# Optimization experiments

Hardware: AMD Instinct MI355X
Metric: run time of the kernel (lower is better)

Reference implementation:

```python
import jax, jax.numpy as jnp
import numpy as np


def _keras_lstm_cell(x, h_tm1, c_tm1, k, rk, b):
    # Keras LSTMCell math: gates ordered i, f, c(g), o
    z = x @ k + h_tm1 @ rk + b  # [B, 4H]
    i, f, g, o = jnp.split(z, 4, axis=-1)
    i = jax.nn.sigmoid(i)
    f = jax.nn.sigmoid(f)
    c = f * c_tm1 + i * jnp.tanh(g)
    h = jax.nn.sigmoid(o) * jnp.tanh(c)
    return h, c


def setup_inputs() -> dict:
    key = jax.random.key(0)
    k1, k2, k3, k4 = jax.random.split(key, 4)
    T, B, H, L = 30, 256, 1024, 4
    inputs = jax.random.normal(k1, (T, B, H), dtype=jnp.float32)
    # scale weights to avoid gate saturation across 30 steps
    kernel = jax.random.normal(k2, (L, H, 4 * H), dtype=jnp.float32) * 0.05
    rec_kernel = jax.random.normal(k3, (L, H, 4 * H), dtype=jnp.float32) * 0.05
    bias = jax.random.normal(k4, (L, 4 * H), dtype=jnp.float32) * 0.05
    return {"inputs": inputs, "kernel": kernel, "rec_kernel": rec_kernel, "bias": bias}


def reference(inputs, kernel, rec_kernel, bias):
    # Faithful to the TF source: it passes (c, h) where Keras expects (h, c),
    # a self-consistent swap across steps, EXCEPT `cur_input = h` actually
    # feeds the Keras cell state c to the next layer. We reproduce that.
    T, B, H = inputs.shape
    L = kernel.shape[0]
    h0 = jnp.zeros((L, B, H), dtype=inputs.dtype)  # keras hidden per layer
    c0 = jnp.zeros((L, B, H), dtype=inputs.dtype)  # keras cell per layer

    def step(carry, x_t):
        hs, cs = carry
        cur = x_t
        new_h, new_c = [], []
        for j in range(L):
            h_new, c_new = _keras_lstm_cell(cur, hs[j], cs[j], kernel[j], rec_kernel[j], bias[j])
            cur = c_new  # source feeds its "h" (== keras cell state) onward
            new_h.append(h_new)
            new_c.append(c_new)
        return (jnp.stack(new_h), jnp.stack(new_c)), cur

    (_, _), outs = jax.lax.scan(step, (h0, c0), inputs)
    return outs[-1]  # final cur_input after the last timestep, shape [B, H]
```

## Files before the change

### kernel.cpp

```cpp
#include <hip/hip_runtime.h>
#include <hip/hip_fp16.h>

typedef _Float16 half8 __attribute__((ext_vector_type(8)));
typedef float floatx4 __attribute__((ext_vector_type(4)));

#define T_STEPS 30
#define BATCH   256
#define HID     1024
#define LAYERS  4
#define N4H     4096
#define K2      2048

#define BM 128
#define BN 128
#define BKH 64
#define KITERS 16
#define ZLD 132

#define AS1(p) ((const __attribute__((address_space(1))) void*)(p))
#define AS3(p) ((__attribute__((address_space(3))) void*)(p))

__global__ void transpose_weights(const float* __restrict__ src_all,
                                  _Float16* __restrict__ wrt, int mat) {
    __shared__ float tile[2][64][65];
    const int j = blockIdx.z;
    const float* src = src_all + (size_t)j * HID * N4H;
    _Float16* dst = wrt + (size_t)j * N4H * K2 + mat * HID;
    const int c0 = blockIdx.x * 64;
    const int k0 = blockIdx.y * 128;
    const int t = threadIdx.x;
    const int c4 = (t & 15) * 4, lr = t >> 4;
    #pragma unroll
    for (int tt = 0; tt < 2; ++tt)
        #pragma unroll
        for (int i = 0; i < 4; ++i) {
            const float4 v = *(const float4*)(src + (size_t)(k0 + tt * 64 + lr + i * 16) * N4H + c0 + c4);
            volatile float* tw = &tile[tt][lr + i * 16][c4];
            tw[0] = v.x; tw[1] = v.y; tw[2] = v.z; tw[3] = v.w;
        }
    __syncthreads();
    const int kg = t & 7, cl0 = t >> 3;
    #pragma unroll
    for (int tt = 0; tt < 2; ++tt)
        #pragma unroll
        for (int i = 0; i < 2; ++i) {
            const int cp = cl0 + i * 32;
            const int c = c0 + cp;
            const int q = ((c & (HID - 1)) << 2) | (c >> 10);
            half8 v;
            #pragma unroll
            for (int jj = 0; jj < 8; ++jj)
                v[jj] = (_Float16)tile[tt][kg * 8 + jj][cp];
            *(half8*)(dst + (size_t)q * K2 + k0 + tt * 64 + kg * 8) = v;
        }
}

__global__ void cvt_inputs(const float* __restrict__ in, _Float16* __restrict__ out) {
    const size_t i = ((size_t)blockIdx.x * 256 + threadIdx.x) * 8;
    const float4 a = *(const float4*)(in + i);
    const float4 b = *(const float4*)(in + i + 4);
    half8 v;
    v[0] = (_Float16)a.x; v[1] = (_Float16)a.y; v[2] = (_Float16)a.z; v[3] = (_Float16)a.w;
    v[4] = (_Float16)b.x; v[5] = (_Float16)b.y; v[6] = (_Float16)b.z; v[7] = (_Float16)b.w;
    *(half8*)(out + i) = v;
}

__global__ __launch_bounds__(512) void lstm_diag(
    const _Float16* __restrict__ Xf,
    _Float16*       __restrict__ c_act,
    _Float16*       __restrict__ h_act,
    const _Float16* __restrict__ WRt,
    const float*    __restrict__ bias,
    float*          __restrict__ c_master,
    int diag, int packed_t, int packed_j)
{
    const int z = blockIdx.z;
    const int t = (packed_t >> (8 * z)) & 255;
    const int j = (packed_j >> (8 * z)) & 255;
    const size_t BH = (size_t)BATCH * HID;

    const _Float16* X    = (j == 0) ? (Xf + (size_t)t * BH)
                                    : (c_act + ((size_t)((diag - 1) & 1) * LAYERS + (j - 1)) * BH);
    const _Float16* Hrec = h_act + (size_t)j * BH;
    const _Float16* WR   = WRt + (size_t)j * N4H * K2;
    const float* bias_j  = bias + (size_t)j * N4H;
    float* c_m           = c_master + (size_t)j * BH;
    _Float16* c_out      = c_act + ((size_t)(diag & 1) * LAYERS + j) * BH;
    _Float16* h_out      = h_act + (size_t)j * BH;

    __shared__ __align__(16) char smem[131072];
    float* zs = (float*)smem;

    const int tid  = threadIdx.x;
    const int w    = tid >> 6, lane = tid & 63;
    const int quad = lane >> 4, l16 = lane & 15;
    const int h    = w >> 2;
    const int sp   = w & 3;
    const int mw   = (sp & 1) * 64;
    const int nw   = (sp >> 1) * 64;
    const int m0   = blockIdx.y * BM;
    const int q0   = blockIdx.x * BN;
    const int th   = tid & 255;
    const int wbase = (w & 3) * 64;

    const _Float16* Ag0 = h ? Hrec : X;
    const _Float16* Bg0 = WR + h * HID;

    floatx4 acc[4][4];
    #pragma unroll
    for (int a = 0; a < 4; ++a)
        #pragma unroll
        for (int b = 0; b < 4; ++b)
            #pragma unroll
            for (int e = 0; e < 4; ++e) acc[a][b][e] = 0.f;

#define STAGE(bufsel, kc_) do {                                                         \
        _Float16* As_ = (_Float16*)(smem + (bufsel) * 65536 + h * 32768);               \
        _Float16* Bs_ = As_ + 8192;                                                     \
        const _Float16* Agk = Ag0 + (kc_);                                              \
        const _Float16* Bgk = Bg0 + (kc_);                                              \
        _Pragma("unroll")                                                               \
        for (int i_ = 0; i_ < 4; ++i_) {                                                \
            const int slot = i_ * 256 + th;                                             \
            const int r_ = slot >> 3;                                                   \
            const int g_ = (slot & 7) ^ (r_ & 7);                                       \
            __builtin_amdgcn_global_load_lds(AS1(Agk + (size_t)(m0 + r_) * HID + g_ * 8),\
                                             AS3(As_ + (i_ * 256 + wbase) * 8), 16, 0, 0);\
        }                                                                               \
        _Pragma("unroll")                                                               \
        for (int i_ = 0; i_ < 4; ++i_) {                                                \
            const int slot = i_ * 256 + th;                                             \
            const int q_ = slot >> 3;                                                   \
            const int g_ = (slot & 7) ^ (q_ & 7);                                       \
            __builtin_amdgcn_global_load_lds(AS1(Bgk + (size_t)(q0 + q_) * K2 + g_ * 8), \
                                             AS3(Bs_ + (i_ * 256 + wbase) * 8), 16, 0, 0);\
        }                                                                               \
    } while (0)

#define COMPUTE(bufsel) do {                                                            \
        const _Float16* As_ = (const _Float16*)(smem + (bufsel) * 65536 + h * 32768);   \
        const _Float16* Bs_ = As_ + 8192;                                               \
        _Pragma("unroll")                                                               \
        for (int ks = 0; ks < 2; ++ks) {                                                \
            const int gq = ks * 4 + quad;                                               \
            half8 bfrag[4];                                                             \
            _Pragma("unroll")                                                           \
            for (int b = 0; b < 4; ++b) {                                               \
                const int q = nw + b * 16 + l16;                                        \
                bfrag[b] = *(const half8*)&Bs_[((q << 3) + (gq ^ (q & 7))) * 8];        \
            }                                                                           \
            _Pragma("unroll")                                                           \
            for (int a = 0; a < 4; ++a) {                                               \
                const int r = mw + a * 16 + l16;                                        \
                const half8 afrag = *(const half8*)&As_[((r << 3) + (gq ^ (r & 7))) * 8];\
                acc[a][0] = __builtin_amdgcn_mfma_f32_16x16x32_f16(afrag, bfrag[0], acc[a][0], 0, 0, 0);\
                acc[a][1] = __builtin_amdgcn_mfma_f32_16x16x32_f16(afrag, bfrag[1], acc[a][1], 0, 0, 0);\
                acc[a][2] = __builtin_amdgcn_mfma_f32_16x16x32_f16(afrag, bfrag[2], acc[a][2], 0, 0, 0);\
                acc[a][3] = __builtin_amdgcn_mfma_f32_16x16x32_f16(afrag, bfrag[3], acc[a][3], 0, 0, 0);\
            }                                                                           \
        }                                                                               \
    } while (0)

    STAGE(0, 0);
    __syncthreads();
    #pragma unroll 2
    for (int ts = 0; ts < KITERS; ++ts) {
        const int cur = ts & 1;
        if (ts + 1 < KITERS) STAGE(cur ^ 1, (ts + 1) * BKH);
        COMPUTE(cur);
        __syncthreads();
    }

    if (h == 0) {
        #pragma unroll
        for (int a = 0; a < 4; ++a)
            #pragma unroll
            for (int b = 0; b < 4; ++b)
                #pragma unroll
                for (int e = 0; e < 4; ++e)
                    zs[(mw + a * 16 + quad * 4 + e) * ZLD + nw + b * 16 + l16] = acc[a][b][e];
    }
    __syncthreads();
    if (h == 1) {
        #pragma unroll
        for (int a = 0; a < 4; ++a)
            #pragma unroll
            for (int b = 0; b < 4; ++b)
                #pragma unroll
                for (int e = 0; e < 4; ++e)
                    zs[(mw + a * 16 + quad * 4 + e) * ZLD + nw + b * 16 + l16] += acc[a][b][e];
    }
    __syncthreads();

    const int nl = tid & 31;
    const int mb = tid >> 5;
    const int n  = blockIdx.x * 32 + nl;
    const float bi = bias_j[n];
    const float bf = bias_j[HID + n];
    const float bg = bias_j[2 * HID + n];
    const float bo = bias_j[3 * HID + n];
    #pragma unroll
    for (int mi = 0; mi < 8; ++mi) {
        const int ml = mb + mi * 16;
        const int m  = m0 + ml;
        const float4 z4 = *(const float4*)&zs[ml * ZLD + 4 * nl];
        const float zi = z4.x + bi;
        const float zf = z4.y + bf;
        const float zg = z4.z + bg;
        const float zo = z4.w + bo;
        const float ig = 1.f / (1.f + __expf(-zi));
        const float fg = 1.f / (1.f + __expf(-zf));
        const float gg = tanhf(zg);
        const float og = 1.f / (1.f + __expf(-zo));
        const size_t idx = (size_t)m * HID + n;
        const float c = fg * c_m[idx] + ig * gg;
        const float hh = og * tanhf(c);
        c_m[idx] = c;
        c_out[idx] = (_Float16)c;
        h_out[idx] = (_Float16)hh;
    }
#undef STAGE
#undef COMPUTE
}

extern "C" void kernel_launch(void* const* d_in, const int* in_sizes, int n_in,
                              void* d_out, int out_size, void* d_ws, size_t ws_size,
                              hipStream_t stream) {
    const float* inputs     = (const float*)d_in[0];
    const float* kernel_    = (const float*)d_in[1];
    const float* rec_kernel = (const float*)d_in[2];
    const float* bias       = (const float*)d_in[3];
    float* out = (float*)d_out;

    char* ws = (char*)d_ws;
    _Float16* WRt      = (_Float16*)(ws);
    _Float16* Xf       = (_Float16*)(ws + 67108864);
    float*    c_master = (float*)   (ws + 82837504);
    _Float16* c_f16    = (_Float16*)(ws + 87031808);
    _Float16* h_f16    = (_Float16*)(ws + 91226112);

    const size_t BH = (size_t)BATCH * HID;

    hipMemsetAsync(c_master, 0, LAYERS * BH * sizeof(float), stream);
    hipMemsetAsync(h_f16, 0, LAYERS * BH * sizeof(_Float16), stream);

    transpose_weights<<<dim3(N4H / 64, HID / 128, LAYERS), 256, 0, stream>>>(
        kernel_, WRt, 0);
    transpose_weights<<<dim3(N4H / 64, HID / 128, LAYERS), 256, 0, stream>>>(
        rec_kernel, WRt, 1);
    cvt_inputs<<<(T_STEPS * BATCH * HID) / 8 / 256, 256, 0, stream>>>(inputs, Xf);

    for (int d = 0; d < T_STEPS + LAYERS - 1; ++d) {
        const int jlo = (d - (T_STEPS - 1)) > 0 ? (d - (T_STEPS - 1)) : 0;
        const int jhi = d < (LAYERS - 1) ? d : (LAYERS - 1);
        const int nc  = jhi - jlo + 1;
        int pt = 0, pj = 0;
        for (int zz = 0; zz < nc; ++zz) {
            const int jj = jlo + zz, tt = d - jj;
            pt |= tt << (8 * zz);
            pj |= jj << (8 * zz);
        }
        lstm_diag<<<dim3(N4H / BN, BATCH / BM, nc), 512, 0, stream>>>(
            Xf, c_f16, h_f16, WRt, bias, c_master, d, pt, pj);
    }

    hipMemcpyAsync(out, c_master + 3 * BH, BH * sizeof(float),
                   hipMemcpyDeviceToDevice, stream);
}
```

Measured before the change: 1.092 ms.

## Split K-tile staging into halves with vmcnt-gated barriers and k-major LDS layout

Splits each 64-wide K tile load into two halves and interleaves them with two compute sub-steps. Partial s_waitcnt vmcnt plus raw barriers replace full __syncthreads, so in-flight global-to-LDS loads can overlap MFMA work at finer granularity. The LDS layout also changes from XOR-swizzled row-major to a k-group-major layout with no swizzle. That simplifies addressing but may introduce LDS bank conflicts, and the hand-tuned waitcnt counts must exactly match the number of outstanding loads.

```diff
diff --git a/kernel.cpp b/kernel.cpp
--- a/kernel.cpp
+++ b/kernel.cpp
@@ -114,62 +114,71 @@
             #pragma unroll
             for (int e = 0; e < 4; ++e) acc[a][b][e] = 0.f;
 
-#define STAGE(bufsel, kc_) do {                                                         \
+#define STAGE_HALF(bufsel, kc_, hb) do {                                                \
         _Float16* As_ = (_Float16*)(smem + (bufsel) * 65536 + h * 32768);               \
         _Float16* Bs_ = As_ + 8192;                                                     \
         const _Float16* Agk = Ag0 + (kc_);                                              \
         const _Float16* Bgk = Bg0 + (kc_);                                              \
         _Pragma("unroll")                                                               \
-        for (int i_ = 0; i_ < 4; ++i_) {                                                \
-            const int slot = i_ * 256 + th;                                             \
-            const int r_ = slot >> 3;                                                   \
-            const int g_ = (slot & 7) ^ (r_ & 7);                                       \
-            __builtin_amdgcn_global_load_lds(AS1(Agk + (size_t)(m0 + r_) * HID + g_ * 8),\
+        for (int i_ = 2 * (hb); i_ < 2 * (hb) + 2; ++i_) {                              \
+            const int s_ = i_ * 256 + th;                                               \
+            const int r_ = s_ & 127, gl_ = s_ >> 7;                                     \
+            __builtin_amdgcn_global_load_lds(AS1(Agk + (size_t)(m0 + r_) * HID + gl_ * 8),\
                                              AS3(As_ + (i_ * 256 + wbase) * 8), 16, 0, 0);\
         }                                                                               \
         _Pragma("unroll")                                                               \
-        for (int i_ = 0; i_ < 4; ++i_) {                                                \
-            const int slot = i_ * 256 + th;                                             \
-            const int q_ = slot >> 3;                                                   \
-            const int g_ = (slot & 7) ^ (q_ & 7);                                       \
-            __builtin_amdgcn_global_load_lds(AS1(Bgk + (size_t)(q0 + q_) * K2 + g_ * 8), \
+        for (int i_ = 2 * (hb); i_ < 2 * (hb) + 2; ++i_) {                              \
+            const int s_ = i_ * 256 + th;                                               \
+            const int q_ = s_ & 127, gl_ = s_ >> 7;                                     \
+            __builtin_amdgcn_global_load_lds(AS1(Bgk + (size_t)(q0 + q_) * K2 + gl_ * 8),\
                                              AS3(Bs_ + (i_ * 256 + wbase) * 8), 16, 0, 0);\
         }                                                                               \
     } while (0)
 
-#define COMPUTE(bufsel) do {                                                            \
+#define COMPUTE_KS(bufsel, ks) do {                                                     \
         const _Float16* As_ = (const _Float16*)(smem + (bufsel) * 65536 + h * 32768);   \
         const _Float16* Bs_ = As_ + 8192;                                               \
-        _Pragma("unroll")                                                               \
-        for (int ks = 0; ks < 2; ++ks) {                                                \
-            const int gq = ks * 4 + quad;                                               \
-            half8 bfrag[4];                                                             \
-            _Pragma("unroll")                                                           \
-            for (int b = 0; b < 4; ++b) {                                               \
-                const int q = nw + b * 16 + l16;                                        \
-                bfrag[b] = *(const half8*)&Bs_[((q << 3) + (gq ^ (q & 7))) * 8];        \
-            }                                                                           \
-            _Pragma("unroll")                                                           \
-            for (int a = 0; a < 4; ++a) {                                               \
-                const int r = mw + a * 16 + l16;                                        \
-                const half8 afrag = *(const half8*)&As_[((r << 3) + (gq ^ (r & 7))) * 8];\
-                acc[a][0] = __builtin_amdgcn_mfma_f32_16x16x32_f16(afrag, bfrag[0], acc[a][0], 0, 0, 0);\
-                acc[a][1] = __builtin_amdgcn_mfma_f32_16x16x32_f16(afrag, bfrag[1], acc[a][1], 0, 0, 0);\
-                acc[a][2] = __builtin_amdgcn_mfma_f32_16x16x32_f16(afrag, bfrag[2], acc[a][2], 0, 0, 0);\
-                acc[a][3] = __builtin_amdgcn_mfma_f32_16x16x32_f16(afrag, bfrag[3], acc[a][3], 0, 0, 0);\
-            }                                                                           \
+        const int lg = (ks) * 4 + quad;                                                 \
+        half8 bfrag[4];                                                                 \
+        _Pragma("unroll")                                                               \
+        for (int b = 0; b < 4; ++b)                                                     \
+            bfrag[b] = *(const half8*)&Bs_[(lg * 128 + nw + b * 16 + l16) * 8];         \
+        _Pragma("unroll")                                                               \
+        for (int a = 0; a < 4; ++a) {                                                   \
+            const half8 afrag = *(const half8*)&As_[(lg * 128 + mw + a * 16 + l16) * 8];\
+            acc[a][0] = __builtin_amdgcn_mfma_f32_16x16x32_f16(afrag, bfrag[0], acc[a][0], 0, 0, 0);\
+            acc[a][1] = __builtin_amdgcn_mfma_f32_16x16x32_f16(afrag, bfrag[1], acc[a][1], 0, 0, 0);\
+            acc[a][2] = __builtin_amdgcn_mfma_f32_16x16x32_f16(afrag, bfrag[2], acc[a][2], 0, 0, 0);\
+            acc[a][3] = __builtin_amdgcn_mfma_f32_16x16x32_f16(afrag, bfrag[3], acc[a][3], 0, 0, 0);\
         }                                                                               \
     } while (0)
 
-    STAGE(0, 0);
-    __syncthreads();
+#define PHASE(WAITN)                                                                    \
+        asm volatile("s_waitcnt vmcnt(" #WAITN ")" ::: "memory");                       \
+        __builtin_amdgcn_s_barrier();                                                   \
+        __builtin_amdgcn_sched_barrier(0);
+
+    STAGE_HALF(0, 0, 0);
+    STAGE_HALF(0, 0, 1);
+
     #pragma unroll 2
-    for (int ts = 0; ts < KITERS; ++ts) {
-        const int cur = ts & 1;
-        if (ts + 1 < KITERS) STAGE(cur ^ 1, (ts + 1) * BKH);
-        COMPUTE(cur);
-        __syncthreads();
-    }
+    for (int ts = 0; ts < KITERS - 1; ++ts) {
+        const int cur = ts & 1, nxt = cur ^ 1;
+        const int kcn = (ts + 1) * BKH;
+        PHASE(4)
+        STAGE_HALF(nxt, kcn, 0);
+        COMPUTE_KS(cur, 0);
+        PHASE(4)
+        STAGE_HALF(nxt, kcn, 1);
+        COMPUTE_KS(cur, 1);
+    }
+    {
+        PHASE(4)
+        COMPUTE_KS(1, 0);
+        PHASE(0)
+        COMPUTE_KS(1, 1);
+    }
+    __syncthreads();
 
     if (h == 0) {
         #pragma unroll
@@ -219,8 +228,9 @@
         c_out[idx] = (_Float16)c;
         h_out[idx] = (_Float16)hh;
     }
-#undef STAGE
-#undef COMPUTE
+#undef STAGE_HALF
+#undef COMPUTE_KS
+#undef PHASE
 }
 
 extern "C" void kernel_launch(void* const* d_in, const int* in_sizes, int n_in,
```

Measured after the change: 1.627 ms. 1.49x slower.

## Shrink N tile to 64 and drop intra-block split-K for more blocks

Applied to the files above, without the earlier changes.

The N tile shrinks from 128 to 64 columns. The two-half split-K, where wave groups reduced the x- and h-halves separately, is replaced by all 8 waves iterating over the full concatenated K=2048, each wave owning a 32x32 output sub-tile. This removes the LDS reduction pass and cuts shared memory from 128KB to 48KB, with launch bounds requesting 4 blocks per CU. The goal is to launch twice as many blocks per diagonal step so more CUs are busy. The cost is more K iterations per block, less data reuse per loaded tile, and reliance on the host grid being sized from BN.

```diff
diff --git a/kernel.cpp b/kernel.cpp
--- a/kernel.cpp
+++ b/kernel.cpp
@@ -12,10 +12,10 @@
 #define K2      2048
 
 #define BM 128
-#define BN 128
-#define BKH 64
-#define KITERS 16
-#define ZLD 132
+#define BN 64
+#define BK 64
+#define KITERS 32
+#define ZLD 68
 
 #define AS1(p) ((const __attribute__((address_space(1))) void*)(p))
 #define AS3(p) ((__attribute__((address_space(3))) void*)(p))
@@ -65,7 +65,7 @@
     *(half8*)(out + i) = v;
 }
 
-__global__ __launch_bounds__(512) void lstm_diag(
+__global__ __launch_bounds__(512, 4) void lstm_diag(
     const _Float16* __restrict__ Xf,
     _Float16*       __restrict__ c_act,
     _Float16*       __restrict__ h_act,
@@ -88,75 +88,65 @@
     _Float16* c_out      = c_act + ((size_t)(diag & 1) * LAYERS + j) * BH;
     _Float16* h_out      = h_act + (size_t)j * BH;
 
-    __shared__ __align__(16) char smem[131072];
+    __shared__ __align__(16) char smem[49152];
     float* zs = (float*)smem;
 
     const int tid  = threadIdx.x;
     const int w    = tid >> 6, lane = tid & 63;
     const int quad = lane >> 4, l16 = lane & 15;
-    const int h    = w >> 2;
-    const int sp   = w & 3;
-    const int mw   = (sp & 1) * 64;
-    const int nw   = (sp >> 1) * 64;
+    const int mw   = (w & 3) * 32;
+    const int nw   = (w >> 2) * 32;
     const int m0   = blockIdx.y * BM;
     const int q0   = blockIdx.x * BN;
-    const int th   = tid & 255;
-    const int wbase = (w & 3) * 64;
-
-    const _Float16* Ag0 = h ? Hrec : X;
-    const _Float16* Bg0 = WR + h * HID;
-
-    floatx4 acc[4][4];
-    #pragma unroll
-    for (int a = 0; a < 4; ++a)
-        #pragma unroll
-        for (int b = 0; b < 4; ++b)
+
+    floatx4 acc[2][2];
+    #pragma unroll
+    for (int a = 0; a < 2; ++a)
+        #pragma unroll
+        for (int b = 0; b < 2; ++b)
             #pragma unroll
             for (int e = 0; e < 4; ++e) acc[a][b][e] = 0.f;
 
 #define STAGE(bufsel, kc_) do {                                                         \
-        _Float16* As_ = (_Float16*)(smem + (bufsel) * 65536 + h * 32768);               \
+        _Float16* As_ = (_Float16*)(smem + (bufsel) * 24576);                           \
         _Float16* Bs_ = As_ + 8192;                                                     \
-        const _Float16* Agk = Ag0 + (kc_);                                              \
-        const _Float16* Bgk = Bg0 + (kc_);                                              \
+        const _Float16* Agk = ((kc_) < HID) ? (X + (kc_)) : (Hrec + ((kc_) - HID));     \
+        const _Float16* Bgk = WR + (kc_);                                               \
         _Pragma("unroll")                                                               \
-        for (int i_ = 0; i_ < 4; ++i_) {                                                \
-            const int slot = i_ * 256 + th;                                             \
+        for (int i_ = 0; i_ < 2; ++i_) {                                                \
+            const int slot = i_ * 512 + tid;                                            \
             const int r_ = slot >> 3;                                                   \
             const int g_ = (slot & 7) ^ (r_ & 7);                                       \
             __builtin_amdgcn_global_load_lds(AS1(Agk + (size_t)(m0 + r_) * HID + g_ * 8),\
-                                             AS3(As_ + (i_ * 256 + wbase) * 8), 16, 0, 0);\
+                                             AS3(As_ + (i_ * 512 + w * 64) * 8), 16, 0, 0);\
         }                                                                               \
-        _Pragma("unroll")                                                               \
-        for (int i_ = 0; i_ < 4; ++i_) {                                                \
-            const int slot = i_ * 256 + th;                                             \
+        {                                                                               \
+            const int slot = tid;                                                       \
             const int q_ = slot >> 3;                                                   \
             const int g_ = (slot & 7) ^ (q_ & 7);                                       \
             __builtin_amdgcn_global_load_lds(AS1(Bgk + (size_t)(q0 + q_) * K2 + g_ * 8), \
-                                             AS3(Bs_ + (i_ * 256 + wbase) * 8), 16, 0, 0);\
+                                             AS3(Bs_ + (w * 64) * 8), 16, 0, 0);        \
         }                                                                               \
     } while (0)
 
 #define COMPUTE(bufsel) do {                                                            \
-        const _Float16* As_ = (const _Float16*)(smem + (bufsel) * 65536 + h * 32768);   \
+        const _Float16* As_ = (const _Float16*)(smem + (bufsel) * 24576);               \
         const _Float16* Bs_ = As_ + 8192;                                               \
         _Pragma("unroll")                                                               \
         for (int ks = 0; ks < 2; ++ks) {                                                \
             const int gq = ks * 4 + quad;                                               \
-            half8 bfrag[4];                                                             \
+            half8 bfrag[2];                                                             \
             _Pragma("unroll")                                                           \
-            for (int b = 0; b < 4; ++b) {                                               \
+            for (int b = 0; b < 2; ++b) {                                               \
                 const int q = nw + b * 16 + l16;                                        \
                 bfrag[b] = *(const half8*)&Bs_[((q << 3) + (gq ^ (q & 7))) * 8];        \
             }                                                                           \
             _Pragma("unroll")                                                           \
-            for (int a = 0; a < 4; ++a) {                                               \
+            for (int a = 0; a < 2; ++a) {                                               \
                 const int r = mw + a * 16 + l16;                                        \
                 const half8 afrag = *(const half8*)&As_[((r << 3) + (gq ^ (r & 7))) * 8];\
                 acc[a][0] = __builtin_amdgcn_mfma_f32_16x16x32_f16(afrag, bfrag[0], acc[a][0], 0, 0, 0);\
                 acc[a][1] = __builtin_amdgcn_mfma_f32_16x16x32_f16(afrag, bfrag[1], acc[a][1], 0, 0, 0);\
-                acc[a][2] = __builtin_amdgcn_mfma_f32_16x16x32_f16(afrag, bfrag[2], acc[a][2], 0, 0, 0);\
-                acc[a][3] = __builtin_amdgcn_mfma_f32_16x16x32_f16(afrag, bfrag[3], acc[a][3], 0, 0, 0);\
             }                                                                           \
         }                                                                               \
     } while (0)
@@ -166,42 +156,30 @@
     #pragma unroll 2
     for (int ts = 0; ts < KITERS; ++ts) {
         const int cur = ts & 1;
-        if (ts + 1 < KITERS) STAGE(cur ^ 1, (ts + 1) * BKH);
+        if (ts + 1 < KITERS) STAGE(cur ^ 1, (ts + 1) * BK);
         COMPUTE(cur);
         __syncthreads();
     }
 
-    if (h == 0) {
-        #pragma unroll
-        for (int a = 0; a < 4; ++a)
+    #pragma unroll
+    for (int a = 0; a < 2; ++a)
+        #pragma unroll
+        for (int b = 0; b < 2; ++b)
             #pragma unroll
-            for (int b = 0; b < 4; ++b)
-                #pragma unroll
-                for (int e = 0; e < 4; ++e)
-                    zs[(mw + a * 16 + quad * 4 + e) * ZLD + nw + b * 16 + l16] = acc[a][b][e];
-    }
+            for (int e = 0; e < 4; ++e)
+                zs[(mw + a * 16 + quad * 4 + e) * ZLD + nw + b * 16 + l16] = acc[a][b][e];
     __syncthreads();
-    if (h == 1) {
-        #pragma unroll
-        for (int a = 0; a < 4; ++a)
-            #pragma unroll
-            for (int b = 0; b < 4; ++b)
-                #pragma unroll
-                for (int e = 0; e < 4; ++e)
-                    zs[(mw + a * 16 + quad * 4 + e) * ZLD + nw + b * 16 + l16] += acc[a][b][e];
-    }
-    __syncthreads();
-
-    const int nl = tid & 31;
-    const int mb = tid >> 5;
-    const int n  = blockIdx.x * 32 + nl;
+
+    const int nl = tid & 15;
+    const int mb = tid >> 4;
+    const int n  = blockIdx.x * 16 + nl;
     const float bi = bias_j[n];
     const float bf = bias_j[HID + n];
     const float bg = bias_j[2 * HID + n];
     const float bo = bias_j[3 * HID + n];
     #pragma unroll
-    for (int mi = 0; mi < 8; ++mi) {
-        const int ml = mb + mi * 16;
+    for (int mi = 0; mi < 4; ++mi) {
+        const int ml = mb + mi * 32;
         const int m  = m0 + ml;
         const float4 z4 = *(const float4*)&zs[ml * ZLD + 4 * nl];
         const float zi = z4.x + bi;
```

Result: slower. 1.140 ms (+4.4%).
